# Kernel tuning notes

Measured on AMD Instinct MI355X. Metric: run time of the kernel, lower is better.

## Reference

```python
import jax, jax.numpy as jnp
import numpy as np

UB = 35.0      # per-coordinate upper bound
SUM = 150.0    # equality constraint sum(z) = 150
NEG_SLOPE = 0.2


def _qp_project_one(v):
    """Solve min_z 0.5||z||^2 - v^T z  s.t. 0<=z<=UB, sum(z)=SUM  (n=5).
    Solution: z_i = clip(v_i - nu, 0, UB) with nu s.t. sum(z)=SUM.
    Exact closed form via the piecewise-linear breakpoints of g(nu)=sum(clip(v-nu,0,UB)).
    This matches QPFunction(Q=I, p=x, G,h box, A,b simplex) with v = -x."""
    bp = jnp.concatenate([v, v - UB])              # [10] breakpoints of g(nu)
    bs = jnp.sort(bp)[::-1]                        # descending in nu; g nondecreasing
    mid = 0.5 * (bs[:-1] + bs[1:])                 # [9] segment midpoints
    free = (v[None, :] > mid[:, None]) & (v[None, :] < mid[:, None] + UB)
    upper = v[None, :] >= mid[:, None] + UB
    nfree = jnp.sum(free, axis=1)
    num = jnp.sum(jnp.where(free, v[None, :], 0.0), axis=1) + UB * jnp.sum(upper, axis=1) - SUM
    nu_cand = num / jnp.maximum(nfree, 1)
    valid = (nfree > 0) & (nu_cand <= bs[:-1] + 1e-6) & (nu_cand >= bs[1:] - 1e-6)
    nu = nu_cand[jnp.argmax(valid)]
    return jnp.clip(v - nu, 0.0, UB)


def setup_inputs() -> dict:
    key = jax.random.key(0)
    ks = jax.random.split(key, 7)
    B, S, A = 65536, 17, 5
    state = jax.random.normal(ks[0], (B, S), dtype=jnp.float32)
    W1 = jax.random.normal(ks[1], (400, S), dtype=jnp.float32) * 0.05
    b1 = jax.random.normal(ks[2], (400,), dtype=jnp.float32) * 0.05
    W2 = jax.random.normal(ks[3], (300, 400), dtype=jnp.float32) * 0.05
    b2 = jax.random.normal(ks[4], (300,), dtype=jnp.float32) * 0.05
    W3 = jax.random.normal(ks[5], (A, 300), dtype=jnp.float32) * 0.05
    b3 = jax.random.normal(ks[6], (A,), dtype=jnp.float32) * 0.05
    return {"state": state, "W1": W1, "b1": b1, "W2": W2, "b2": b2,
            "W3": W3, "b3": b3, "training": 0}


def reference(state, W1, b1, W2, b2, W3, b3, training):
    lrelu = lambda x: jax.nn.leaky_relu(x, NEG_SLOPE)
    a = lrelu(state @ W1.T + b1)
    a = lrelu(a @ W2.T + b2)
    scaled_a = lrelu(a @ W3.T + b3)            # [B, 5]
    # QPFunction is called with linear term p = scaled_a, so v = -scaled_a
    opt_a = jax.vmap(_qp_project_one)(-scaled_a)
    return opt_a
```

## Files before the change

### kernel.cpp

```cpp
#include <hip/hip_runtime.h>
#include <hip/hip_bf16.h>

typedef __bf16 bf16x8 __attribute__((ext_vector_type(8)));
typedef float  f32x4  __attribute__((ext_vector_type(4)));

#define UBV   35.0f
#define SUMC  150.0f

__device__ __forceinline__ float lrelu(float x) { return fmaxf(x, 0.2f * x); }

__device__ __forceinline__ unsigned pk8(float a, float b) {
    return ((unsigned)__builtin_amdgcn_cvt_pk_fp8_f32(a, b, 0, false)) & 0xffffu;
}
__device__ __forceinline__ long mk64(unsigned lo, unsigned hi) {
    return (long)(((unsigned long long)hi << 32) | (unsigned long long)lo);
}
__device__ __forceinline__ void async16(void* lds_uniform, const void* gsrc) {
    __builtin_amdgcn_global_load_lds(
        (__attribute__((address_space(1))) void*)(gsrc),
        (__attribute__((address_space(3))) void*)(lds_uniform),
        16, 0, 0);
}


__global__ void prep_kernel(const float* __restrict__ W1, const float* __restrict__ b1,
                            const float* __restrict__ W2, const float* __restrict__ b2,
                            const float* __restrict__ W3, const float* __restrict__ b3,
                            __bf16* __restrict__ w1p, uint2* __restrict__ w2p,
                            uint2* __restrict__ w3c)
{
    int idx = blockIdx.x * blockDim.x + threadIdx.x;
    if (idx < 1664) {
        int lane = idx & 63;
        int nt = idx >> 6;
        int c16 = lane & 15, g = lane >> 4;
        int kk = nt >> 1, hh = nt & 1;
        int kap = kk * 32 + (c16 >> 2) * 8 + hh * 4 + (c16 & 3);
        bf16x8 v;
        #pragma unroll
        for (int j = 0; j < 8; ++j) {
            int k = g * 8 + j;
            float x = 0.f;
            if (kap < 400) {
                if (k < 17) x = W1[kap * 17 + k];
                else if (k == 17) x = b1[kap];
            } else if (kap == 400) {
                if (k == 17) x = 1.0f;
            }
            v[j] = (__bf16)x;
        }
        *(bf16x8*)(w1p + idx * 8) = v;
    } else if (idx < 1664 + 16640) {
        int i2 = idx - 1664;
        int fg = i2 >> 6, lane = i2 & 63;
        int q = fg / 65, rem = fg % 65;
        int t = rem / 13, kt = rem % 13;
        int c16 = lane & 15, g = lane >> 4;
        int local = t * 16 + c16;
        int ff = q * 79 + local;
        float v[8];
        #pragma unroll
        for (int j = 0; j < 8; ++j) {
            int kap = kt * 32 + g * 8 + j;
            float x = 0.f;
            if (local == 79) {
                x = (kap == 400) ? 1.0f : 0.f;
            } else if (local < 79 && ff < 300) {
                if (kap < 400) x = W2[ff * 400 + kap];
                else if (kap == 400) x = b2[ff];
            }
            v[j] = x;
        }
        uint2 d;
        d.x = pk8(v[0], v[1]) | (pk8(v[2], v[3]) << 16);
        d.y = pk8(v[4], v[5]) | (pk8(v[6], v[7]) << 16);
        w2p[i2] = d;
    } else if (idx < 1664 + 16640 + 768) {
        int i3 = idx - 1664 - 16640;
        int fg = i3 >> 6, lane = i3 & 63;
        int q = fg / 3, k2 = fg % 3;
        int o = lane & 15, g = lane >> 4;
        float v[8];
        #pragma unroll
        for (int j = 0; j < 8; ++j) {
            int t2  = 2 * k2 + (j >> 2);
            int rho = g * 4 + (j & 3);
            int local = t2 * 16 + rho;
            float x = 0.f;
            if (o < 5 && t2 < 5) {
                if (local == 79) x = b3[o] * 0.25f;
                else if (local < 79 && q * 79 + local < 300)
                    x = W3[o * 300 + q * 79 + local];
            }
            v[j] = x;
        }
        uint2 d;
        d.x = pk8(v[0], v[1]) | (pk8(v[2], v[3]) << 16);
        d.y = pk8(v[4], v[5]) | (pk8(v[6], v[7]) << 16);
        w3c[i3] = d;
    }
}

__global__ __launch_bounds__(256, 1)
void actor_kernel(const float* __restrict__ state,
                  const __bf16* __restrict__ w1p,
                  const uint2* __restrict__ w2p,
                  const uint2* __restrict__ w3c,
                  float* __restrict__ out)
{
    __shared__ __align__(16) char s_mem[2][33792];

    const int tid = threadIdx.x;
    const int wid = tid >> 6;
    const int ln  = tid & 63;
    const int g   = ln >> 4, c16 = ln & 15;
    const int brow = blockIdx.x << 7;

    {
        const char* gb1 = (const char*)w1p;
        #pragma unroll
        for (int i = wid; i < 26; i += 4)
            async16(&s_mem[0][0] + i * 1024, gb1 + i * 1024 + ln * 16);
        const char* gb2 = (const char*)w2p;
        #pragma unroll
        for (int i = wid; i < 33; i += 4)
            async16(&s_mem[1][0] + i * 1024, gb2 + i * 1024 + ln * 16);
    }

    bf16x8 sbA, sbB;
    {
        const float* spA = state + (brow + wid * 32 + c16) * 17;
        const float* spB = spA + 16 * 17;
        if (g == 0) {
            #pragma unroll
            for (int j = 0; j < 8; ++j) { sbA[j] = (__bf16)spA[j]; sbB[j] = (__bf16)spB[j]; }
        } else if (g == 1) {
            #pragma unroll
            for (int j = 0; j < 8; ++j) { sbA[j] = (__bf16)spA[8 + j]; sbB[j] = (__bf16)spB[8 + j]; }
        } else if (g == 2) {
            sbA[0] = (__bf16)spA[16]; sbB[0] = (__bf16)spB[16];
            sbA[1] = (__bf16)1.0f;    sbB[1] = (__bf16)1.0f;
            #pragma unroll
            for (int j = 2; j < 8; ++j) { sbA[j] = (__bf16)0.f; sbB[j] = (__bf16)0.f; }
        } else {
            #pragma unroll
            for (int j = 0; j < 8; ++j) { sbA[j] = (__bf16)0.f; sbB[j] = (__bf16)0.f; }
        }
    }

    __syncthreads();

    long frvA[13], frvB[13];
    #pragma unroll
    for (int kt = 0; kt < 13; ++kt) {
        bf16x8 we = *(const bf16x8*)(&s_mem[0][0] + ((2 * kt) * 64 + ln) * 16);
        bf16x8 wo = *(const bf16x8*)(&s_mem[0][0] + ((2 * kt + 1) * 64 + ln) * 16);
        f32x4 aeA = {0.f,0.f,0.f,0.f}, aoA = {0.f,0.f,0.f,0.f};
        f32x4 aeB = {0.f,0.f,0.f,0.f}, aoB = {0.f,0.f,0.f,0.f};
        aeA = __builtin_amdgcn_mfma_f32_16x16x32_bf16(we, sbA, aeA, 0, 0, 0);
        aoA = __builtin_amdgcn_mfma_f32_16x16x32_bf16(wo, sbA, aoA, 0, 0, 0);
        aeB = __builtin_amdgcn_mfma_f32_16x16x32_bf16(we, sbB, aeB, 0, 0, 0);
        aoB = __builtin_amdgcn_mfma_f32_16x16x32_bf16(wo, sbB, aoB, 0, 0, 0);
        frvA[kt] = mk64(
            pk8(lrelu(aeA[0]), lrelu(aeA[1])) | (pk8(lrelu(aeA[2]), lrelu(aeA[3])) << 16),
            pk8(lrelu(aoA[0]), lrelu(aoA[1])) | (pk8(lrelu(aoA[2]), lrelu(aoA[3])) << 16));
        frvB[kt] = mk64(
            pk8(lrelu(aeB[0]), lrelu(aeB[1])) | (pk8(lrelu(aeB[2]), lrelu(aeB[3])) << 16),
            pk8(lrelu(aoB[0]), lrelu(aoB[1])) | (pk8(lrelu(aoB[2]), lrelu(aoB[3])) << 16));
    }

    __syncthreads();

    f32x4 ccsA = {0.f, 0.f, 0.f, 0.f};
    f32x4 ccsB = {0.f, 0.f, 0.f, 0.f};
    const long* gw3 = (const long*)w3c;

    #pragma unroll 1
    for (int q = 0; q < 4; ++q) {
        if (q < 3) {
            char* lb = &s_mem[q & 1][0];
            const char* gb = (const char*)w2p + (q + 1) * 33280;
            #pragma unroll
            for (int i = wid; i < 33; i += 4)
                async16(lb + i * 1024, gb + i * 1024 + ln * 16);
        }
        long w3q0 = gw3[(q * 3 + 0) * 64 + ln];
        long w3q1 = gw3[(q * 3 + 1) * 64 + ln];
        long w3q2 = gw3[(q * 3 + 2) * 64 + ln];

        const long* wq = (const long*)(&s_mem[(q & 1) ^ 1][0]);
        f32x4 aA0 = {0.f,0.f,0.f,0.f}, aA1 = {0.f,0.f,0.f,0.f}, aA2 = {0.f,0.f,0.f,0.f};
        f32x4 aA3 = {0.f,0.f,0.f,0.f}, aA4 = {0.f,0.f,0.f,0.f};
        f32x4 aB0 = {0.f,0.f,0.f,0.f}, aB1 = {0.f,0.f,0.f,0.f}, aB2 = {0.f,0.f,0.f,0.f};
        f32x4 aB3 = {0.f,0.f,0.f,0.f}, aB4 = {0.f,0.f,0.f,0.f};
        #pragma unroll
        for (int kt = 0; kt < 13; ++kt) {
            long f0 = wq[(0 * 13 + kt) * 64 + ln];
            long f1 = wq[(1 * 13 + kt) * 64 + ln];
            long f2 = wq[(2 * 13 + kt) * 64 + ln];
            long f3 = wq[(3 * 13 + kt) * 64 + ln];
            long f4 = wq[(4 * 13 + kt) * 64 + ln];
            aA0 = __builtin_amdgcn_mfma_f32_16x16x32_fp8_fp8(f0, frvA[kt], aA0, 0, 0, 0);
            aB0 = __builtin_amdgcn_mfma_f32_16x16x32_fp8_fp8(f0, frvB[kt], aB0, 0, 0, 0);
            aA1 = __builtin_amdgcn_mfma_f32_16x16x32_fp8_fp8(f1, frvA[kt], aA1, 0, 0, 0);
            aB1 = __builtin_amdgcn_mfma_f32_16x16x32_fp8_fp8(f1, frvB[kt], aB1, 0, 0, 0);
            aA2 = __builtin_amdgcn_mfma_f32_16x16x32_fp8_fp8(f2, frvA[kt], aA2, 0, 0, 0);
            aB2 = __builtin_amdgcn_mfma_f32_16x16x32_fp8_fp8(f2, frvB[kt], aB2, 0, 0, 0);
            aA3 = __builtin_amdgcn_mfma_f32_16x16x32_fp8_fp8(f3, frvA[kt], aA3, 0, 0, 0);
            aB3 = __builtin_amdgcn_mfma_f32_16x16x32_fp8_fp8(f3, frvB[kt], aB3, 0, 0, 0);
            aA4 = __builtin_amdgcn_mfma_f32_16x16x32_fp8_fp8(f4, frvA[kt], aA4, 0, 0, 0);
            aB4 = __builtin_amdgcn_mfma_f32_16x16x32_fp8_fp8(f4, frvB[kt], aB4, 0, 0, 0);
        }
        {
            unsigned d0 = pk8(lrelu(aA0[0]), lrelu(aA0[1])) | (pk8(lrelu(aA0[2]), lrelu(aA0[3])) << 16);
            unsigned d1 = pk8(lrelu(aA1[0]), lrelu(aA1[1])) | (pk8(lrelu(aA1[2]), lrelu(aA1[3])) << 16);
            unsigned d2 = pk8(lrelu(aA2[0]), lrelu(aA2[1])) | (pk8(lrelu(aA2[2]), lrelu(aA2[3])) << 16);
            unsigned d3 = pk8(lrelu(aA3[0]), lrelu(aA3[1])) | (pk8(lrelu(aA3[2]), lrelu(aA3[3])) << 16);
            unsigned d4 = pk8(lrelu(aA4[0]), lrelu(aA4[1])) | (pk8(lrelu(aA4[2]), lrelu(aA4[3])) << 16);
            f32x4 cc = {0.f, 0.f, 0.f, 0.f};
            cc = __builtin_amdgcn_mfma_f32_16x16x32_fp8_fp8(w3q0, mk64(d0, d1), cc, 0, 0, 0);
            cc = __builtin_amdgcn_mfma_f32_16x16x32_fp8_fp8(w3q1, mk64(d2, d3), cc, 0, 0, 0);
            cc = __builtin_amdgcn_mfma_f32_16x16x32_fp8_fp8(w3q2, mk64(d4, 0u),  cc, 0, 0, 0);
            ccsA += cc;
        }
        {
            unsigned d0 = pk8(lrelu(aB0[0]), lrelu(aB0[1])) | (pk8(lrelu(aB0[2]), lrelu(aB0[3])) << 16);
            unsigned d1 = pk8(lrelu(aB1[0]), lrelu(aB1[1])) | (pk8(lrelu(aB1[2]), lrelu(aB1[3])) << 16);
            unsigned d2 = pk8(lrelu(aB2[0]), lrelu(aB2[1])) | (pk8(lrelu(aB2[2]), lrelu(aB2[3])) << 16);
            unsigned d3 = pk8(lrelu(aB3[0]), lrelu(aB3[1])) | (pk8(lrelu(aB3[2]), lrelu(aB3[3])) << 16);
            unsigned d4 = pk8(lrelu(aB4[0]), lrelu(aB4[1])) | (pk8(lrelu(aB4[2]), lrelu(aB4[3])) << 16);
            f32x4 cc = {0.f, 0.f, 0.f, 0.f};
            cc = __builtin_amdgcn_mfma_f32_16x16x32_fp8_fp8(w3q0, mk64(d0, d1), cc, 0, 0, 0);
            cc = __builtin_amdgcn_mfma_f32_16x16x32_fp8_fp8(w3q1, mk64(d2, d3), cc, 0, 0, 0);
            cc = __builtin_amdgcn_mfma_f32_16x16x32_fp8_fp8(w3q2, mk64(d4, 0u),  cc, 0, 0, 0);
            ccsB += cc;
        }
        if (q < 3) __syncthreads();
    }

    float tA4 = __shfl_xor(ccsA[0], 16);
    float sB0 = __shfl_xor(ccsB[0], 16);
    float sB1 = __shfl_xor(ccsB[1], 16);
    float sB2 = __shfl_xor(ccsB[2], 16);
    float sB3 = __shfl_xor(ccsB[3], 16);

    if (ln < 32) {
        float v[5];
        if (ln < 16) {
            v[0] = -lrelu(ccsA[0]); v[1] = -lrelu(ccsA[1]);
            v[2] = -lrelu(ccsA[2]); v[3] = -lrelu(ccsA[3]);
            v[4] = -lrelu(tA4);
        } else {
            v[0] = -lrelu(sB0); v[1] = -lrelu(sB1);
            v[2] = -lrelu(sB2); v[3] = -lrelu(sB3);
            v[4] = -lrelu(ccsB[0]);
        }

        float bp[10];
        #pragma unroll
        for (int i = 0; i < 5; ++i) { bp[i] = v[i]; bp[i + 5] = v[i] - UBV; }
        float blo = -1e30f, glo = 0.f;
        #pragma unroll
        for (int j = 0; j < 10; ++j) {
            float b = bp[j];
            float gsum = 0.f;
            #pragma unroll
            for (int i = 0; i < 5; ++i) {
                float zc = v[i] - b;
                zc = fminf(fmaxf(zc, 0.f), UBV);
                gsum += zc;
            }
            if (gsum >= SUMC && b > blo) { blo = b; glo = gsum; }
        }
        float bhi = 1e30f;
        #pragma unroll
        for (int j = 0; j < 10; ++j) {
            float b = bp[j];
            if (b > blo && b < bhi) bhi = b;
        }
        float mid = 0.5f * (blo + bhi);
        int nfree = 0;
        #pragma unroll
        for (int i = 0; i < 5; ++i)
            nfree += (v[i] > mid && v[i] < mid + UBV) ? 1 : 0;
        float nu = (nfree > 0) ? blo + (glo - SUMC) / (float)nfree : blo;

        int row = brow + wid * 32 + ln;
        #pragma unroll
        for (int o = 0; o < 5; ++o) {
            float zf = v[o] - nu;
            zf = fminf(fmaxf(zf, 0.f), UBV);
            out[row * 5 + o] = zf;
        }
    }
}

extern "C" void kernel_launch(void* const* d_in, const int* in_sizes, int n_in,
                              void* d_out, int out_size, void* d_ws, size_t ws_size,
                              hipStream_t stream) {
    const float* state = (const float*)d_in[0];
    const float* W1    = (const float*)d_in[1];
    const float* b1    = (const float*)d_in[2];
    const float* W2    = (const float*)d_in[3];
    const float* b2    = (const float*)d_in[4];
    const float* W3    = (const float*)d_in[5];
    const float* b3    = (const float*)d_in[6];
    float* out = (float*)d_out;

    char* base = (char*)d_ws;
    __bf16* w1p = (__bf16*)base;
    uint2*  w2p = (uint2*)(base + 26624);
    uint2*  w3c = (uint2*)(base + 26624 + 133120);

    const int total = 1664 + 16640 + 768;
    prep_kernel<<<(total + 255) / 256, 256, 0, stream>>>(W1, b1, W2, b2, W3, b3,
                                                         w1p, w2p, w3c);

    int B = in_sizes[0] / 17;
    actor_kernel<<<B / 128, 256, 0, stream>>>(state, w1p, w2p, w3c, out);
}
```

Before: 29.96 us.

## Interleave W2 fragments for 128-bit LDS reads and reorder layer-2 MFMA loop

The prep kernel now writes W2 tiles so that consecutive k-tile pairs are adjacent per lane. The main kernel can then fetch two fp8 fragments with one 16-byte LDS read instead of two 8-byte reads. The layer-2 loop now runs per output tile instead of interleaving five accumulators, which cuts live accumulator registers but makes each tile's MFMA chain serially dependent. W3 fragments are also preloaded into registers once before the loop, and fp8 packing uses the word-select form of cvt_pk_fp8 to drop the shift/or masking.

```diff
diff --git a/kernel.cpp b/kernel.cpp
--- a/kernel.cpp
+++ b/kernel.cpp
@@ -3,14 +3,17 @@
 
 typedef __bf16 bf16x8 __attribute__((ext_vector_type(8)));
 typedef float  f32x4  __attribute__((ext_vector_type(4)));
+typedef long   long2v __attribute__((ext_vector_type(2)));
 
 #define UBV   35.0f
 #define SUMC  150.0f
 
 __device__ __forceinline__ float lrelu(float x) { return fmaxf(x, 0.2f * x); }
 
-__device__ __forceinline__ unsigned pk8(float a, float b) {
-    return ((unsigned)__builtin_amdgcn_cvt_pk_fp8_f32(a, b, 0, false)) & 0xffffu;
+__device__ __forceinline__ unsigned pkword(float a, float b, float c, float d) {
+    unsigned w = (unsigned)__builtin_amdgcn_cvt_pk_fp8_f32(a, b, 0, false);
+    w = (unsigned)__builtin_amdgcn_cvt_pk_fp8_f32(c, d, (int)w, true);
+    return w;
 }
 __device__ __forceinline__ long mk64(unsigned lo, unsigned hi) {
     return (long)(((unsigned long long)hi << 32) | (unsigned long long)lo);
@@ -72,9 +75,11 @@
             v[j] = x;
         }
         uint2 d;
-        d.x = pk8(v[0], v[1]) | (pk8(v[2], v[3]) << 16);
-        d.y = pk8(v[4], v[5]) | (pk8(v[6], v[7]) << 16);
-        w2p[i2] = d;
+        d.x = pkword(v[0], v[1], v[2], v[3]);
+        d.y = pkword(v[4], v[5], v[6], v[7]);
+        int within = (kt < 12) ? ((kt >> 1) * 128 + lane * 2 + (kt & 1))
+                               : (768 + lane);
+        w2p[(q * 5 + t) * 832 + within] = d;
     } else if (idx < 1664 + 16640 + 768) {
         int i3 = idx - 1664 - 16640;
         int fg = i3 >> 6, lane = i3 & 63;
@@ -95,8 +100,8 @@
             v[j] = x;
         }
         uint2 d;
-        d.x = pk8(v[0], v[1]) | (pk8(v[2], v[3]) << 16);
-        d.y = pk8(v[4], v[5]) | (pk8(v[6], v[7]) << 16);
+        d.x = pkword(v[0], v[1], v[2], v[3]);
+        d.y = pkword(v[4], v[5], v[6], v[7]);
         w3c[i3] = d;
     }
 }
@@ -146,6 +151,16 @@
             #pragma unroll
             for (int j = 0; j < 8; ++j) { sbA[j] = (__bf16)0.f; sbB[j] = (__bf16)0.f; }
         }
+    }
+
+    long w3r[4][3];
+    {
+        const long* gw3 = (const long*)w3c;
+        #pragma unroll
+        for (int q = 0; q < 4; ++q)
+            #pragma unroll
+            for (int k2 = 0; k2 < 3; ++k2)
+                w3r[q][k2] = gw3[(q * 3 + k2) * 64 + ln];
     }
 
     __syncthreads();
@@ -162,18 +177,17 @@
         aeB = __builtin_amdgcn_mfma_f32_16x16x32_bf16(we, sbB, aeB, 0, 0, 0);
         aoB = __builtin_amdgcn_mfma_f32_16x16x32_bf16(wo, sbB, aoB, 0, 0, 0);
         frvA[kt] = mk64(
-            pk8(lrelu(aeA[0]), lrelu(aeA[1])) | (pk8(lrelu(aeA[2]), lrelu(aeA[3])) << 16),
-            pk8(lrelu(aoA[0]), lrelu(aoA[1])) | (pk8(lrelu(aoA[2]), lrelu(aoA[3])) << 16));
+            pkword(lrelu(aeA[0]), lrelu(aeA[1]), lrelu(aeA[2]), lrelu(aeA[3])),
+            pkword(lrelu(aoA[0]), lrelu(aoA[1]), lrelu(aoA[2]), lrelu(aoA[3])));
         frvB[kt] = mk64(
-            pk8(lrelu(aeB[0]), lrelu(aeB[1])) | (pk8(lrelu(aeB[2]), lrelu(aeB[3])) << 16),
-            pk8(lrelu(aoB[0]), lrelu(aoB[1])) | (pk8(lrelu(aoB[2]), lrelu(aoB[3])) << 16));
+            pkword(lrelu(aeB[0]), lrelu(aeB[1]), lrelu(aeB[2]), lrelu(aeB[3])),
+            pkword(lrelu(aoB[0]), lrelu(aoB[1]), lrelu(aoB[2]), lrelu(aoB[3])));
     }
 
     __syncthreads();
 
     f32x4 ccsA = {0.f, 0.f, 0.f, 0.f};
     f32x4 ccsB = {0.f, 0.f, 0.f, 0.f};
-    const long* gw3 = (const long*)w3c;
 
     #pragma unroll 1
     for (int q = 0; q < 4; ++q) {
@@ -184,55 +198,39 @@
             for (int i = wid; i < 33; i += 4)
                 async16(lb + i * 1024, gb + i * 1024 + ln * 16);
         }
-        long w3q0 = gw3[(q * 3 + 0) * 64 + ln];
-        long w3q1 = gw3[(q * 3 + 1) * 64 + ln];
-        long w3q2 = gw3[(q * 3 + 2) * 64 + ln];
-
-        const long* wq = (const long*)(&s_mem[(q & 1) ^ 1][0]);
-        f32x4 aA0 = {0.f,0.f,0.f,0.f}, aA1 = {0.f,0.f,0.f,0.f}, aA2 = {0.f,0.f,0.f,0.f};
-        f32x4 aA3 = {0.f,0.f,0.f,0.f}, aA4 = {0.f,0.f,0.f,0.f};
-        f32x4 aB0 = {0.f,0.f,0.f,0.f}, aB1 = {0.f,0.f,0.f,0.f}, aB2 = {0.f,0.f,0.f,0.f};
-        f32x4 aB3 = {0.f,0.f,0.f,0.f}, aB4 = {0.f,0.f,0.f,0.f};
-        #pragma unroll
-        for (int kt = 0; kt < 13; ++kt) {
-            long f0 = wq[(0 * 13 + kt) * 64 + ln];
-            long f1 = wq[(1 * 13 + kt) * 64 + ln];
-            long f2 = wq[(2 * 13 + kt) * 64 + ln];
-            long f3 = wq[(3 * 13 + kt) * 64 + ln];
-            long f4 = wq[(4 * 13 + kt) * 64 + ln];
-            aA0 = __builtin_amdgcn_mfma_f32_16x16x32_fp8_fp8(f0, frvA[kt], aA0, 0, 0, 0);
-            aB0 = __builtin_amdgcn_mfma_f32_16x16x32_fp8_fp8(f0, frvB[kt], aB0, 0, 0, 0);
-            aA1 = __builtin_amdgcn_mfma_f32_16x16x32_fp8_fp8(f1, frvA[kt], aA1, 0, 0, 0);
-            aB1 = __builtin_amdgcn_mfma_f32_16x16x32_fp8_fp8(f1, frvB[kt], aB1, 0, 0, 0);
-            aA2 = __builtin_amdgcn_mfma_f32_16x16x32_fp8_fp8(f2, frvA[kt], aA2, 0, 0, 0);
-            aB2 = __builtin_amdgcn_mfma_f32_16x16x32_fp8_fp8(f2, frvB[kt], aB2, 0, 0, 0);
-            aA3 = __builtin_amdgcn_mfma_f32_16x16x32_fp8_fp8(f3, frvA[kt], aA3, 0, 0, 0);
-            aB3 = __builtin_amdgcn_mfma_f32_16x16x32_fp8_fp8(f3, frvB[kt], aB3, 0, 0, 0);
-            aA4 = __builtin_amdgcn_mfma_f32_16x16x32_fp8_fp8(f4, frvA[kt], aA4, 0, 0, 0);
-            aB4 = __builtin_amdgcn_mfma_f32_16x16x32_fp8_fp8(f4, frvB[kt], aB4, 0, 0, 0);
+
+        const char* bufp = &s_mem[(q & 1) ^ 1][0];
+        unsigned wdA[5], wdB[5];
+        #pragma unroll
+        for (int t = 0; t < 5; ++t) {
+            const char* bt = bufp + t * 6656;
+            f32x4 aA = {0.f,0.f,0.f,0.f}, aB = {0.f,0.f,0.f,0.f};
+            #pragma unroll
+            for (int kt2 = 0; kt2 < 6; ++kt2) {
+                long2v p = *(const long2v*)(bt + kt2 * 1024 + ln * 16);
+                aA = __builtin_amdgcn_mfma_f32_16x16x32_fp8_fp8(p[0], frvA[2 * kt2],     aA, 0, 0, 0);
+                aB = __builtin_amdgcn_mfma_f32_16x16x32_fp8_fp8(p[0], frvB[2 * kt2],     aB, 0, 0, 0);
+                aA = __builtin_amdgcn_mfma_f32_16x16x32_fp8_fp8(p[1], frvA[2 * kt2 + 1], aA, 0, 0, 0);
+                aB = __builtin_amdgcn_mfma_f32_16x16x32_fp8_fp8(p[1], frvB[2 * kt2 + 1], aB, 0, 0, 0);
+            }
+            long p12 = *(const long*)(bt + 6144 + ln * 8);
+            aA = __builtin_amdgcn_mfma_f32_16x16x32_fp8_fp8(p12, frvA[12], aA, 0, 0, 0);
+            aB = __builtin_amdgcn_mfma_f32_16x16x32_fp8_fp8(p12, frvB[12], aB, 0, 0, 0);
+            wdA[t] = pkword(lrelu(aA[0]), lrelu(aA[1]), lrelu(aA[2]), lrelu(aA[3]));
+            wdB[t] = pkword(lrelu(aB[0]), lrelu(aB[1]), lrelu(aB[2]), lrelu(aB[3]));
         }
         {
-            unsigned d0 = pk8(lrelu(aA0[0]), lrelu(aA0[1])) | (pk8(lrelu(aA0[2]), lrelu(aA0[3])) << 16);
-            unsigned d1 = pk8(lrelu(aA1[0]), lrelu(aA1[1])) | (pk8(lrelu(aA1[2]), lrelu(aA1[3])) << 16);
-            unsigned d2 = pk8(lrelu(aA2[0]), lrelu(aA2[1])) | (pk8(lrelu(aA2[2]), lrelu(aA2[3])) << 16);
-            unsigned d3 = pk8(lrelu(aA3[0]), lrelu(aA3[1])) | (pk8(lrelu(aA3[2]), lrelu(aA3[3])) << 16);
-            unsigned d4 = pk8(lrelu(aA4[0]), lrelu(aA4[1])) | (pk8(lrelu(aA4[2]), lrelu(aA4[3])) << 16);
             f32x4 cc = {0.f, 0.f, 0.f, 0.f};
-            cc = __builtin_amdgcn_mfma_f32_16x16x32_fp8_fp8(w3q0, mk64(d0, d1), cc, 0, 0, 0);
-            cc = __builtin_amdgcn_mfma_f32_16x16x32_fp8_fp8(w3q1, mk64(d2, d3), cc, 0, 0, 0);
-            cc = __builtin_amdgcn_mfma_f32_16x16x32_fp8_fp8(w3q2, mk64(d4, 0u),  cc, 0, 0, 0);
+            cc = __builtin_amdgcn_mfma_f32_16x16x32_fp8_fp8(w3r[q][0], mk64(wdA[0], wdA[1]), cc, 0, 0, 0);
+            cc = __builtin_amdgcn_mfma_f32_16x16x32_fp8_fp8(w3r[q][1], mk64(wdA[2], wdA[3]), cc, 0, 0, 0);
+            cc = __builtin_amdgcn_mfma_f32_16x16x32_fp8_fp8(w3r[q][2], mk64(wdA[4], 0u),     cc, 0, 0, 0);
             ccsA += cc;
         }
         {
-            unsigned d0 = pk8(lrelu(aB0[0]), lrelu(aB0[1])) | (pk8(lrelu(aB0[2]), lrelu(aB0[3])) << 16);
-            unsigned d1 = pk8(lrelu(aB1[0]), lrelu(aB1[1])) | (pk8(lrelu(aB1[2]), lrelu(aB1[3])) << 16);
-            unsigned d2 = pk8(lrelu(aB2[0]), lrelu(aB2[1])) | (pk8(lrelu(aB2[2]), lrelu(aB2[3])) << 16);
-            unsigned d3 = pk8(lrelu(aB3[0]), lrelu(aB3[1])) | (pk8(lrelu(aB3[2]), lrelu(aB3[3])) << 16);
-            unsigned d4 = pk8(lrelu(aB4[0]), lrelu(aB4[1])) | (pk8(lrelu(aB4[2]), lrelu(aB4[3])) << 16);
             f32x4 cc = {0.f, 0.f, 0.f, 0.f};
-            cc = __builtin_amdgcn_mfma_f32_16x16x32_fp8_fp8(w3q0, mk64(d0, d1), cc, 0, 0, 0);
-            cc = __builtin_amdgcn_mfma_f32_16x16x32_fp8_fp8(w3q1, mk64(d2, d3), cc, 0, 0, 0);
-            cc = __builtin_amdgcn_mfma_f32_16x16x32_fp8_fp8(w3q2, mk64(d4, 0u),  cc, 0, 0, 0);
+            cc = __builtin_amdgcn_mfma_f32_16x16x32_fp8_fp8(w3r[q][0], mk64(wdB[0], wdB[1]), cc, 0, 0, 0);
+            cc = __builtin_amdgcn_mfma_f32_16x16x32_fp8_fp8(w3r[q][1], mk64(wdB[2], wdB[3]), cc, 0, 0, 0);
+            cc = __builtin_amdgcn_mfma_f32_16x16x32_fp8_fp8(w3r[q][2], mk64(wdB[4], 0u),     cc, 0, 0, 0);
             ccsB += cc;
         }
         if (q < 3) __syncthreads();
```

Result: faster. 28.59 us (-4.6%).
